# Performance work log

Hardware: AMD Instinct MI355X
Metric: run time of the kernel (lower is better)

The kernel has to match this reference:

```python
import jax, jax.numpy as jnp
import numpy as np

NW1, L1 = 4096, 36
NW2, L2 = 1024, 100
D, NHEAD = 128, 8
HD = D // NHEAD
# alternating full / half-full windows -> exact token count
N1 = (NW1 // 2) * (L1 + L1 // 2)   # 110592
N2 = (NW2 // 2) * (L2 + L2 // 2)   # 76800
N = N1 + N2                        # 187392


def _build_group(nw, L, perm, start):
    """Prefix-valid windows: even windows full (L tokens), odd half (L//2)."""
    lens = np.where(np.arange(nw) % 2 == 0, L, L // 2)
    valid = np.arange(L)[None, :] < lens[:, None]          # [nw, L]
    inds = np.zeros((nw, L), np.int32)
    n = int(lens.sum())
    inds[valid] = perm[start:start + n]                    # row-major prefix fill
    return inds, ~valid, start + n


def setup_inputs() -> dict:
    rng = np.random.default_rng(0)
    perm = rng.permutation(N).astype(np.int32)
    inds1, mask1, ptr = _build_group(NW1, L1, perm, 0)
    inds2, mask2, ptr = _build_group(NW2, L2, perm, ptr)
    assert ptr == N
    ks = jax.random.split(jax.random.key(0), 7)
    scale = 1.0 / np.sqrt(D)
    return {
        "feat_2d": jax.random.normal(ks[0], (N, D), jnp.float32),
        "pos1": jax.random.normal(ks[1], (NW1, L1, D), jnp.float32),
        "pos2": jax.random.normal(ks[2], (NW2, L2, D), jnp.float32),
        "in_proj_w": jax.random.normal(ks[3], (3 * D, D), jnp.float32) * scale,
        "in_proj_b": jax.random.normal(ks[4], (3 * D,), jnp.float32) * 0.02,
        "out_proj_w": jax.random.normal(ks[5], (D, D), jnp.float32) * scale,
        "out_proj_b": jax.random.normal(ks[6], (D,), jnp.float32) * 0.02,
        "inds1": jnp.asarray(inds1),
        "inds2": jnp.asarray(inds2),
        "mask1": jnp.asarray(mask1),
        "mask2": jnp.asarray(mask2),
    }


def _mha(qk, v, pad_mask, Wi, bi, Wo, bo):
    """torch.nn.MultiheadAttention math (eval mode, dropout=0).
    qk, v: [nw, L, D]; pad_mask: [nw, L] True=padded key."""
    nw, L, _ = qk.shape
    q = (qk @ Wi[:D].T + bi[:D]).reshape(nw, L, NHEAD, HD)
    k = (qk @ Wi[D:2 * D].T + bi[D:2 * D]).reshape(nw, L, NHEAD, HD)
    vv = (v @ Wi[2 * D:].T + bi[2 * D:]).reshape(nw, L, NHEAD, HD)
    scores = jnp.einsum('nqhd,nkhd->nhqk', q, k) * (HD ** -0.5)
    scores = jnp.where(pad_mask[:, None, None, :],
                       jnp.finfo(scores.dtype).min, scores)
    attn = jax.nn.softmax(scores, axis=-1)
    out = jnp.einsum('nhqk,nkhd->nqhd', attn, vv).reshape(nw, L, D)
    return out @ Wo.T + bo


def reference(feat_2d, pos1, pos2, in_proj_w, in_proj_b, out_proj_w,
              out_proj_b, inds1, inds2, mask1, mask2):
    out = jnp.zeros_like(feat_2d)
    for inds, mask, pos in ((inds1, mask1, pos1), (inds2, mask2, pos2)):
        f = feat_2d[inds]                      # flat2window gather [nw, L, D]
        o = _mha(f + pos, f, mask,
                 in_proj_w, in_proj_b, out_proj_w, out_proj_b)
        o = o * (~mask)[..., None]             # zero padded slots
        out = out.at[inds.reshape(-1)].add(o.reshape(-1, D))  # window2flat
    return out
```

## Files before the change

### kernel.cpp

```cpp
#include <hip/hip_runtime.h>

typedef __attribute__((ext_vector_type(4))) float f32x4;
typedef __attribute__((ext_vector_type(8))) short short8;
typedef __attribute__((ext_vector_type(4))) short short4v;

#define MFMA_B16(a,b,c) __builtin_amdgcn_mfma_f32_16x16x32_bf16((a),(b),(c),0,0,0)

static __device__ __forceinline__ unsigned short f2bf(float x){
  unsigned int u = __float_as_uint(x);
  u += 0x7fffu + ((u >> 16) & 1u);
  return (unsigned short)(u >> 16);
}

static __device__ __forceinline__ short8 pack8(f32x4 a, f32x4 b){
  short8 r;
  r[0]=(short)f2bf(a[0]); r[1]=(short)f2bf(a[1]); r[2]=(short)f2bf(a[2]); r[3]=(short)f2bf(a[3]);
  r[4]=(short)f2bf(b[0]); r[5]=(short)f2bf(b[1]); r[6]=(short)f2bf(b[2]); r[7]=(short)f2bf(b[3]);
  return r;
}

static __device__ __forceinline__ short4v pack4(const f32x4& a){
  short4v r;
  r[0]=(short)f2bf(a[0]); r[1]=(short)f2bf(a[1]); r[2]=(short)f2bf(a[2]); r[3]=(short)f2bf(a[3]);
  return r;
}

__global__ void prep_w(const float* __restrict__ ipw, const float* __restrict__ opw,
                       unsigned short* __restrict__ wbf){
  int i = blockIdx.x * 256 + threadIdx.x;
  float v = (i < 384*128) ? ipw[i] : opw[i - 384*128];
  wbf[i] = f2bf(v);
}

#define STR 136

template<int TTP>
__global__ __launch_bounds__(256, 2)
void fused_attn(const float* __restrict__ feat,
                const float* __restrict__ pos,
                const int* __restrict__ inds,
                int LW,
                const unsigned short* __restrict__ wqkv,
                const unsigned short* __restrict__ wout,
                const float* __restrict__ ipb, const float* __restrict__ opb,
                float* __restrict__ out)
{
  constexpr int PSTR = 16*(TTP+1) + 8;
  constexpr int STRT = 24;
  constexpr int KOFF = 16*TTP;
  extern __shared__ __align__(16) unsigned short smem[];
  unsigned short* sQK = smem;
  unsigned short* sF  = smem + 16*TTP*STR;
  unsigned short* sPb = smem + 2*16*TTP*STR;
  unsigned short* sTs = smem + 2*16*TTP*STR + 4*16*PSTR;

  const int w = blockIdx.x;
  const int Lv = (w & 1) ? (LW >> 1) : LW;
  const int T  = (Lv + 15) >> 4;
  const long ibase = (long)w * LW;
  const int tid = threadIdx.x;
  const int wv = tid >> 6, lane = tid & 63, c = lane & 15, q = lane >> 4;
  const short8 Z8 = {0,0,0,0,0,0,0,0};
  const f32x4  Z4 = {0.f,0.f,0.f,0.f};

  {
    const int rg = tid >> 4, ch = tid & 15;
    #pragma unroll
    for (int s = 0; s < TTP; ++s){
      if (s < T){
        const int row = s*16 + rg;
        short8 fv = Z8, qv = Z8;
        if (row < Lv){
          const int tok = inds[ibase + row];
          const float* fr = feat + (long)tok*128 + ch*8;
          const float* pr = pos + (ibase + row)*128 + ch*8;
          f32x4 f0 = *(const f32x4*)fr, f1 = *(const f32x4*)(fr+4);
          f32x4 p0 = *(const f32x4*)pr, p1 = *(const f32x4*)(pr+4);
          fv = pack8(f0, f1); qv = pack8(f0+p0, f1+p1);
        }
        *(short8*)&sF [row*STR + ch*8] = fv;
        *(short8*)&sQK[row*STR + ch*8] = qv;
      }
    }
  }
  __syncthreads();

  unsigned short* Pb = sPb + wv*16*PSTR;
  unsigned short* Ts = sTs + wv*16*STRT;
  short4v of[2][TTP];

  #pragma unroll
  for (int hh = 0; hh < 2; ++hh){
    const int h = wv*2 + hh;
    short8 bQ[4], bK[4], bV[4];
    const unsigned short* wr = wqkv + (h*16 + c)*128 + q*8;
    #pragma unroll
    for (int kk = 0; kk < 4; ++kk){
      bQ[kk] = *(const short8*)(wr + kk*32);
      bK[kk] = *(const short8*)(wr + kk*32 + 128*128);
      bV[kk] = *(const short8*)(wr + kk*32 + 2*128*128);
    }
    float bq_r[4], bk_r[4];
    #pragma unroll
    for (int r = 0; r < 4; ++r){
      bq_r[r] = ipb[h*16 + 4*q + r];
      bk_r[r] = ipb[128 + h*16 + 4*q + r];
    }
    const float bv_c = ipb[256 + h*16 + c];

    short8 qAf[TTP], kBf[TTP];

    #pragma unroll
    for (int t = 0; t < TTP; ++t) if (t < T){
      f32x4 qt = Z4, kt = Z4, vt = Z4;
      #pragma unroll
      for (int kk = 0; kk < 4; ++kk){
        const short8 aQ = *(const short8*)&sQK[(16*t + c)*STR + kk*32 + q*8];
        const short8 aF = *(const short8*)&sF [(16*t + c)*STR + kk*32 + q*8];
        qt = MFMA_B16(bQ[kk], aQ, qt);
        kt = MFMA_B16(bK[kk], aQ, kt);
        vt = MFMA_B16(aF, bV[kk], vt);
      }
      #pragma unroll
      for (int r = 0; r < 4; ++r){
        qt[r] = (qt[r] + bq_r[r]) * 0.25f;
        kt[r] += bk_r[r];
        const int key = 16*t + 4*q + r;
        vt[r] = (key < Lv) ? (vt[r] + bv_c) : 0.f;
      }
      *(short4v*)&Pb[c*PSTR + 16*t + 4*q]   = pack4(vt);
      *(short4v*)&Ts[c*STRT + 4*q]          = pack4(qt);
      *(short4v*)&Pb[c*PSTR + KOFF + 4*q]   = pack4(kt);
      const short8 qf = *(const short8*)&Ts[c*STRT + q*8];
      const short8 kf = *(const short8*)&Pb[c*PSTR + KOFF + q*8];
      qAf[t] = (q < 2) ? qf : Z8;
      kBf[t] = (q < 2) ? kf : Z8;
    }
    {
      const short4v z4 = {0,0,0,0};
      *(short4v*)&Pb[c*PSTR + KOFF + 4*q] = z4;
    }

    short8 vBf[(TTP+1)/2];
    #pragma unroll
    for (int u = 0; u < (TTP+1)/2; ++u) if (u < ((T+1)>>1))
      vBf[u] = *(const short8*)&Pb[c*PSTR + 32*u + q*8];

    #pragma unroll
    for (int t = 0; t < TTP; ++t) if (t < T){
      f32x4 St[TTP];
      #pragma unroll
      for (int tk = 0; tk < TTP; ++tk) if (tk < T){
        St[tk] = MFMA_B16(kBf[tk], qAf[t], Z4);
        #pragma unroll
        for (int r = 0; r < 4; ++r){
          const int key = 16*tk + 4*q + r;
          if (key >= Lv) St[tk][r] = -1e30f;
        }
      }
      f32x4 mm = {-1e30f,-1e30f,-1e30f,-1e30f};
      #pragma unroll
      for (int tk = 0; tk < TTP; ++tk) if (tk < T){
        mm[0]=fmaxf(mm[0],St[tk][0]); mm[1]=fmaxf(mm[1],St[tk][1]);
        mm[2]=fmaxf(mm[2],St[tk][2]); mm[3]=fmaxf(mm[3],St[tk][3]);
      }
      float m = fmaxf(fmaxf(mm[0],mm[1]), fmaxf(mm[2],mm[3]));
      m = fmaxf(m, __shfl_xor(m, 16));
      m = fmaxf(m, __shfl_xor(m, 32));
      f32x4 ss = Z4;
      #pragma unroll
      for (int tk = 0; tk < TTP; ++tk) if (tk < T){
        #pragma unroll
        for (int r = 0; r < 4; ++r){
          float e = __expf(St[tk][r] - m);
          St[tk][r] = e; ss[r] += e;
        }
      }
      float sum = (ss[0]+ss[1]) + (ss[2]+ss[3]);
      sum += __shfl_xor(sum, 16);
      sum += __shfl_xor(sum, 32);
      const float inv = 1.0f / sum;
      #pragma unroll
      for (int tk = 0; tk < TTP; ++tk) if (tk < T){
        short4v p4;
        #pragma unroll
        for (int r = 0; r < 4; ++r) p4[r] = (short)f2bf(St[tk][r] * inv);
        *(short4v*)&Pb[c*PSTR + 16*tk + 4*q] = p4;
      }
      f32x4 o = Z4;
      #pragma unroll
      for (int u = 0; u < (TTP+1)/2; ++u) if (u < ((T+1)>>1)){
        const short8 ap = *(const short8*)&Pb[c*PSTR + 32*u + q*8];
        o = MFMA_B16(ap, vBf[u], o);
      }
      short4v ob;
      #pragma unroll
      for (int r = 0; r < 4; ++r) ob[r] = (short)f2bf(o[r]);
      of[hh][t] = ob;
    }
  }

  __syncthreads();
  #pragma unroll
  for (int hh = 0; hh < 2; ++hh){
    const int h = wv*2 + hh;
    #pragma unroll
    for (int t = 0; t < TTP; ++t) if (t < T){
      #pragma unroll
      for (int r = 0; r < 4; ++r)
        sF[(16*t + 4*q + r)*STR + h*16 + c] = (unsigned short)of[hh][t][r];
    }
  }
  __syncthreads();

  float bo_r[8];
  #pragma unroll
  for (int ct = 0; ct < 8; ++ct) bo_r[ct] = opb[ct*16 + c];
  #pragma unroll
  for (int ti = 0; ti < 2; ++ti){
    const int t = wv + ti*4;
    if (t < T){
      f32x4 acc[8];
      #pragma unroll
      for (int ct = 0; ct < 8; ++ct) acc[ct] = Z4;
      #pragma unroll
      for (int p = 0; p < 4; ++p){
        const short8 ao = *(const short8*)&sF[(16*t + c)*STR + p*32 + q*8];
        #pragma unroll
        for (int ct = 0; ct < 8; ++ct){
          const short8 bw = *(const short8*)&wout[(ct*16 + c)*128 + p*32 + q*8];
          acc[ct] = MFMA_B16(ao, bw, acc[ct]);
        }
      }
      #pragma unroll
      for (int r = 0; r < 4; ++r){
        const int l = 16*t + 4*q + r;
        if (l < Lv){
          const int tok = inds[ibase + l];
          float* orow = out + (long)tok*128;
          #pragma unroll
          for (int ct = 0; ct < 8; ++ct)
            orow[ct*16 + c] = acc[ct][r] + bo_r[ct];
        }
      }
    }
  }
}

#define TT3 3
#define PSTR3 (16*(TT3+1) + 8)
#define STRT3 24
#define KOFF3 (16*TT3)
#define HALF3 (2*48*STR + 4*16*PSTR3 + 4*16*STRT3)

__global__ __launch_bounds__(512, 4)
void fused_attn3_2w(const float* __restrict__ feat,
                    const float* __restrict__ pos,
                    const int* __restrict__ inds,
                    const unsigned short* __restrict__ wqkv,
                    const unsigned short* __restrict__ wout,
                    const float* __restrict__ ipb, const float* __restrict__ opb,
                    float* __restrict__ out)
{
  extern __shared__ __align__(16) unsigned short smem[];
  const int tid = threadIdx.x;
  const int wv8 = tid >> 6;
  const int wh  = wv8 >> 2;
  const int wv  = wv8 & 3;
  const int lane = tid & 63, c = lane & 15, q = lane >> 4;

  unsigned short* base = smem + wh*HALF3;
  unsigned short* sQK = base;
  unsigned short* sF  = base + 48*STR;
  unsigned short* sPb = base + 2*48*STR;
  unsigned short* sTs = sPb + 4*16*PSTR3;

  const int w = blockIdx.x*2 + wh;
  const int LW = 36;
  const int Lv = wh ? 18 : 36;
  const int T  = wh ? 2 : 3;
  const long ibase = (long)w * LW;
  const short8 Z8 = {0,0,0,0,0,0,0,0};
  const f32x4  Z4 = {0.f,0.f,0.f,0.f};

  {
    const int ltid = tid & 255;
    const int rg = ltid >> 4, ch = ltid & 15;
    #pragma unroll
    for (int s = 0; s < TT3; ++s){
      if (s < T){
        const int row = s*16 + rg;
        short8 fv = Z8, qv = Z8;
        if (row < Lv){
          const int tok = inds[ibase + row];
          const float* fr = feat + (long)tok*128 + ch*8;
          const float* pr = pos + (ibase + row)*128 + ch*8;
          f32x4 f0 = *(const f32x4*)fr, f1 = *(const f32x4*)(fr+4);
          f32x4 p0 = *(const f32x4*)pr, p1 = *(const f32x4*)(pr+4);
          fv = pack8(f0, f1); qv = pack8(f0+p0, f1+p1);
        }
        *(short8*)&sF [row*STR + ch*8] = fv;
        *(short8*)&sQK[row*STR + ch*8] = qv;
      }
    }
  }
  __syncthreads();

  unsigned short* Pb = sPb + wv*16*PSTR3;
  unsigned short* Ts = sTs + wv*16*STRT3;
  short4v of[2][TT3];

  #pragma unroll
  for (int hh = 0; hh < 2; ++hh){
    const int h = wv*2 + hh;
    short8 bQ[4], bK[4], bV[4];
    const unsigned short* wr = wqkv + (h*16 + c)*128 + q*8;
    #pragma unroll
    for (int kk = 0; kk < 4; ++kk){
      bQ[kk] = *(const short8*)(wr + kk*32);
      bK[kk] = *(const short8*)(wr + kk*32 + 128*128);
      bV[kk] = *(const short8*)(wr + kk*32 + 2*128*128);
    }
    float bq_r[4], bk_r[4];
    #pragma unroll
    for (int r = 0; r < 4; ++r){
      bq_r[r] = ipb[h*16 + 4*q + r];
      bk_r[r] = ipb[128 + h*16 + 4*q + r];
    }
    const float bv_c = ipb[256 + h*16 + c];

    short8 qAf[TT3], kBf[TT3];

    #pragma unroll
    for (int t = 0; t < TT3; ++t) if (t < T){
      f32x4 qt = Z4, kt = Z4, vt = Z4;
      #pragma unroll
      for (int kk = 0; kk < 4; ++kk){
        const short8 aQ = *(const short8*)&sQK[(16*t + c)*STR + kk*32 + q*8];
        const short8 aF = *(const short8*)&sF [(16*t + c)*STR + kk*32 + q*8];
        qt = MFMA_B16(bQ[kk], aQ, qt);
        kt = MFMA_B16(bK[kk], aQ, kt);
        vt = MFMA_B16(aF, bV[kk], vt);
      }
      #pragma unroll
      for (int r = 0; r < 4; ++r){
        qt[r] = (qt[r] + bq_r[r]) * 0.25f;
        kt[r] += bk_r[r];
        const int key = 16*t + 4*q + r;
        vt[r] = (key < Lv) ? (vt[r] + bv_c) : 0.f;
      }
      *(short4v*)&Pb[c*PSTR3 + 16*t + 4*q]   = pack4(vt);
      *(short4v*)&Ts[c*STRT3 + 4*q]          = pack4(qt);
      *(short4v*)&Pb[c*PSTR3 + KOFF3 + 4*q]  = pack4(kt);
      const short8 qf = *(const short8*)&Ts[c*STRT3 + q*8];
      const short8 kf = *(const short8*)&Pb[c*PSTR3 + KOFF3 + q*8];
      qAf[t] = (q < 2) ? qf : Z8;
      kBf[t] = (q < 2) ? kf : Z8;
    }
    {
      const short4v z4 = {0,0,0,0};
      *(short4v*)&Pb[c*PSTR3 + KOFF3 + 4*q] = z4;
    }

    short8 vBf[2];
    #pragma unroll
    for (int u = 0; u < 2; ++u) if (u < ((T+1)>>1))
      vBf[u] = *(const short8*)&Pb[c*PSTR3 + 32*u + q*8];

    #pragma unroll
    for (int t = 0; t < TT3; ++t) if (t < T){
      f32x4 St[TT3];
      #pragma unroll
      for (int tk = 0; tk < TT3; ++tk) if (tk < T){
        St[tk] = MFMA_B16(kBf[tk], qAf[t], Z4);
        #pragma unroll
        for (int r = 0; r < 4; ++r){
          const int key = 16*tk + 4*q + r;
          if (key >= Lv) St[tk][r] = -1e30f;
        }
      }
      f32x4 mm = {-1e30f,-1e30f,-1e30f,-1e30f};
      #pragma unroll
      for (int tk = 0; tk < TT3; ++tk) if (tk < T){
        mm[0]=fmaxf(mm[0],St[tk][0]); mm[1]=fmaxf(mm[1],St[tk][1]);
        mm[2]=fmaxf(mm[2],St[tk][2]); mm[3]=fmaxf(mm[3],St[tk][3]);
      }
      float m = fmaxf(fmaxf(mm[0],mm[1]), fmaxf(mm[2],mm[3]));
      m = fmaxf(m, __shfl_xor(m, 16));
      m = fmaxf(m, __shfl_xor(m, 32));
      f32x4 ss = Z4;
      #pragma unroll
      for (int tk = 0; tk < TT3; ++tk) if (tk < T){
        #pragma unroll
        for (int r = 0; r < 4; ++r){
          float e = __expf(St[tk][r] - m);
          St[tk][r] = e; ss[r] += e;
        }
      }
      float sum = (ss[0]+ss[1]) + (ss[2]+ss[3]);
      sum += __shfl_xor(sum, 16);
      sum += __shfl_xor(sum, 32);
      const float inv = 1.0f / sum;
      #pragma unroll
      for (int tk = 0; tk < TT3; ++tk) if (tk < T){
        short4v p4;
        #pragma unroll
        for (int r = 0; r < 4; ++r) p4[r] = (short)f2bf(St[tk][r] * inv);
        *(short4v*)&Pb[c*PSTR3 + 16*tk + 4*q] = p4;
      }
      f32x4 o = Z4;
      #pragma unroll
      for (int u = 0; u < 2; ++u) if (u < ((T+1)>>1)){
        const short8 ap = *(const short8*)&Pb[c*PSTR3 + 32*u + q*8];
        o = MFMA_B16(ap, vBf[u], o);
      }
      short4v ob;
      #pragma unroll
      for (int r = 0; r < 4; ++r) ob[r] = (short)f2bf(o[r]);
      of[hh][t] = ob;
    }
  }

  __syncthreads();
  #pragma unroll
  for (int hh = 0; hh < 2; ++hh){
    const int h = wv*2 + hh;
    #pragma unroll
    for (int t = 0; t < TT3; ++t) if (t < T){
      #pragma unroll
      for (int r = 0; r < 4; ++r)
        sF[(16*t + 4*q + r)*STR + h*16 + c] = (unsigned short)of[hh][t][r];
    }
  }
  __syncthreads();

  {
    const int t = wv;
    if (t < T){
      float bo_r[8];
      #pragma unroll
      for (int ct = 0; ct < 8; ++ct) bo_r[ct] = opb[ct*16 + c];
      f32x4 acc[8];
      #pragma unroll
      for (int ct = 0; ct < 8; ++ct) acc[ct] = Z4;
      #pragma unroll
      for (int p = 0; p < 4; ++p){
        const short8 ao = *(const short8*)&sF[(16*t + c)*STR + p*32 + q*8];
        #pragma unroll
        for (int ct = 0; ct < 8; ++ct){
          const short8 bw = *(const short8*)&wout[(ct*16 + c)*128 + p*32 + q*8];
          acc[ct] = MFMA_B16(ao, bw, acc[ct]);
        }
      }
      #pragma unroll
      for (int r = 0; r < 4; ++r){
        const int l = 16*t + 4*q + r;
        if (l < Lv){
          const int tok = inds[ibase + l];
          float* orow = out + (long)tok*128;
          #pragma unroll
          for (int ct = 0; ct < 8; ++ct)
            orow[ct*16 + c] = acc[ct][r] + bo_r[ct];
        }
      }
    }
  }
}

extern "C" void kernel_launch(void* const* d_in, const int* in_sizes, int n_in,
                              void* d_out, int out_size, void* d_ws, size_t ws_size,
                              hipStream_t stream) {
  const float* feat = (const float*)d_in[0];
  const float* pos1 = (const float*)d_in[1];
  const float* pos2 = (const float*)d_in[2];
  const float* ipw  = (const float*)d_in[3];
  const float* ipb  = (const float*)d_in[4];
  const float* opw  = (const float*)d_in[5];
  const float* opb  = (const float*)d_in[6];
  const int*   inds1 = (const int*)d_in[7];
  const int*   inds2 = (const int*)d_in[8];
  float* out = (float*)d_out;
  unsigned short* wbf = (unsigned short*)d_ws;
  unsigned short* wob = wbf + 384*128;

  prep_w<<<dim3(256), dim3(256), 0, stream>>>(ipw, opw, wbf);

  {
    const int lds2 = (2*112*STR + 4*16*(16*8 + 8) + 4*16*24) * 2;
    hipFuncSetAttribute((const void*)fused_attn<7>,
                        hipFuncAttributeMaxDynamicSharedMemorySize, lds2);
    fused_attn<7><<<dim3(1024), dim3(256), lds2, stream>>>(
        feat, pos2, inds2, 100, wbf, wob, ipb, opb, out);
  }
  {
    const int lds1 = 2*HALF3*2;
    hipFuncSetAttribute((const void*)fused_attn3_2w,
                        hipFuncAttributeMaxDynamicSharedMemorySize, lds1);
    fused_attn3_2w<<<dim3(2048), dim3(512), lds1, stream>>>(
        feat, pos1, inds1, wbf, wob, ipb, opb, out);
  }
}
```

Baseline: 467.6 us.

## Merge both window-group attention kernels into one launch with block-index dispatch

Combines the L=100 group kernel and the paired L=36 group kernel into a single 512-thread kernel whose block index selects the branch. This removes one launch and the tail gap between the two kernels, so both groups can run concurrently on the device. The L=100 branch now runs with 512 threads, but only four waves do the attention, and it uses the larger shared-memory footprint for every block, which may lower occupancy for the L=36 blocks. Register pressure from the merged code under launch_bounds(512,4) is another risk.

```diff
diff --git a/kernel.cpp b/kernel.cpp
--- a/kernel.cpp
+++ b/kernel.cpp
@@ -34,218 +34,9 @@
 
 #define STR 136
 
-template<int TTP>
-__global__ __launch_bounds__(256, 2)
-void fused_attn(const float* __restrict__ feat,
-                const float* __restrict__ pos,
-                const int* __restrict__ inds,
-                int LW,
-                const unsigned short* __restrict__ wqkv,
-                const unsigned short* __restrict__ wout,
-                const float* __restrict__ ipb, const float* __restrict__ opb,
-                float* __restrict__ out)
-{
-  constexpr int PSTR = 16*(TTP+1) + 8;
-  constexpr int STRT = 24;
-  constexpr int KOFF = 16*TTP;
-  extern __shared__ __align__(16) unsigned short smem[];
-  unsigned short* sQK = smem;
-  unsigned short* sF  = smem + 16*TTP*STR;
-  unsigned short* sPb = smem + 2*16*TTP*STR;
-  unsigned short* sTs = smem + 2*16*TTP*STR + 4*16*PSTR;
-
-  const int w = blockIdx.x;
-  const int Lv = (w & 1) ? (LW >> 1) : LW;
-  const int T  = (Lv + 15) >> 4;
-  const long ibase = (long)w * LW;
-  const int tid = threadIdx.x;
-  const int wv = tid >> 6, lane = tid & 63, c = lane & 15, q = lane >> 4;
-  const short8 Z8 = {0,0,0,0,0,0,0,0};
-  const f32x4  Z4 = {0.f,0.f,0.f,0.f};
-
-  {
-    const int rg = tid >> 4, ch = tid & 15;
-    #pragma unroll
-    for (int s = 0; s < TTP; ++s){
-      if (s < T){
-        const int row = s*16 + rg;
-        short8 fv = Z8, qv = Z8;
-        if (row < Lv){
-          const int tok = inds[ibase + row];
-          const float* fr = feat + (long)tok*128 + ch*8;
-          const float* pr = pos + (ibase + row)*128 + ch*8;
-          f32x4 f0 = *(const f32x4*)fr, f1 = *(const f32x4*)(fr+4);
-          f32x4 p0 = *(const f32x4*)pr, p1 = *(const f32x4*)(pr+4);
-          fv = pack8(f0, f1); qv = pack8(f0+p0, f1+p1);
-        }
-        *(short8*)&sF [row*STR + ch*8] = fv;
-        *(short8*)&sQK[row*STR + ch*8] = qv;
-      }
-    }
-  }
-  __syncthreads();
-
-  unsigned short* Pb = sPb + wv*16*PSTR;
-  unsigned short* Ts = sTs + wv*16*STRT;
-  short4v of[2][TTP];
-
-  #pragma unroll
-  for (int hh = 0; hh < 2; ++hh){
-    const int h = wv*2 + hh;
-    short8 bQ[4], bK[4], bV[4];
-    const unsigned short* wr = wqkv + (h*16 + c)*128 + q*8;
-    #pragma unroll
-    for (int kk = 0; kk < 4; ++kk){
-      bQ[kk] = *(const short8*)(wr + kk*32);
-      bK[kk] = *(const short8*)(wr + kk*32 + 128*128);
-      bV[kk] = *(const short8*)(wr + kk*32 + 2*128*128);
-    }
-    float bq_r[4], bk_r[4];
-    #pragma unroll
-    for (int r = 0; r < 4; ++r){
-      bq_r[r] = ipb[h*16 + 4*q + r];
-      bk_r[r] = ipb[128 + h*16 + 4*q + r];
-    }
-    const float bv_c = ipb[256 + h*16 + c];
-
-    short8 qAf[TTP], kBf[TTP];
-
-    #pragma unroll
-    for (int t = 0; t < TTP; ++t) if (t < T){
-      f32x4 qt = Z4, kt = Z4, vt = Z4;
-      #pragma unroll
-      for (int kk = 0; kk < 4; ++kk){
-        const short8 aQ = *(const short8*)&sQK[(16*t + c)*STR + kk*32 + q*8];
-        const short8 aF = *(const short8*)&sF [(16*t + c)*STR + kk*32 + q*8];
-        qt = MFMA_B16(bQ[kk], aQ, qt);
-        kt = MFMA_B16(bK[kk], aQ, kt);
-        vt = MFMA_B16(aF, bV[kk], vt);
-      }
-      #pragma unroll
-      for (int r = 0; r < 4; ++r){
-        qt[r] = (qt[r] + bq_r[r]) * 0.25f;
-        kt[r] += bk_r[r];
-        const int key = 16*t + 4*q + r;
-        vt[r] = (key < Lv) ? (vt[r] + bv_c) : 0.f;
-      }
-      *(short4v*)&Pb[c*PSTR + 16*t + 4*q]   = pack4(vt);
-      *(short4v*)&Ts[c*STRT + 4*q]          = pack4(qt);
-      *(short4v*)&Pb[c*PSTR + KOFF + 4*q]   = pack4(kt);
-      const short8 qf = *(const short8*)&Ts[c*STRT + q*8];
-      const short8 kf = *(const short8*)&Pb[c*PSTR + KOFF + q*8];
-      qAf[t] = (q < 2) ? qf : Z8;
-      kBf[t] = (q < 2) ? kf : Z8;
-    }
-    {
-      const short4v z4 = {0,0,0,0};
-      *(short4v*)&Pb[c*PSTR + KOFF + 4*q] = z4;
-    }
-
-    short8 vBf[(TTP+1)/2];
-    #pragma unroll
-    for (int u = 0; u < (TTP+1)/2; ++u) if (u < ((T+1)>>1))
-      vBf[u] = *(const short8*)&Pb[c*PSTR + 32*u + q*8];
-
-    #pragma unroll
-    for (int t = 0; t < TTP; ++t) if (t < T){
-      f32x4 St[TTP];
-      #pragma unroll
-      for (int tk = 0; tk < TTP; ++tk) if (tk < T){
-        St[tk] = MFMA_B16(kBf[tk], qAf[t], Z4);
-        #pragma unroll
-        for (int r = 0; r < 4; ++r){
-          const int key = 16*tk + 4*q + r;
-          if (key >= Lv) St[tk][r] = -1e30f;
-        }
-      }
-      f32x4 mm = {-1e30f,-1e30f,-1e30f,-1e30f};
-      #pragma unroll
-      for (int tk = 0; tk < TTP; ++tk) if (tk < T){
-        mm[0]=fmaxf(mm[0],St[tk][0]); mm[1]=fmaxf(mm[1],St[tk][1]);
-        mm[2]=fmaxf(mm[2],St[tk][2]); mm[3]=fmaxf(mm[3],St[tk][3]);
-      }
-      float m = fmaxf(fmaxf(mm[0],mm[1]), fmaxf(mm[2],mm[3]));
-      m = fmaxf(m, __shfl_xor(m, 16));
-      m = fmaxf(m, __shfl_xor(m, 32));
-      f32x4 ss = Z4;
-      #pragma unroll
-      for (int tk = 0; tk < TTP; ++tk) if (tk < T){
-        #pragma unroll
-        for (int r = 0; r < 4; ++r){
-          float e = __expf(St[tk][r] - m);
-          St[tk][r] = e; ss[r] += e;
-        }
-      }
-      float sum = (ss[0]+ss[1]) + (ss[2]+ss[3]);
-      sum += __shfl_xor(sum, 16);
-      sum += __shfl_xor(sum, 32);
-      const float inv = 1.0f / sum;
-      #pragma unroll
-      for (int tk = 0; tk < TTP; ++tk) if (tk < T){
-        short4v p4;
-        #pragma unroll
-        for (int r = 0; r < 4; ++r) p4[r] = (short)f2bf(St[tk][r] * inv);
-        *(short4v*)&Pb[c*PSTR + 16*tk + 4*q] = p4;
-      }
-      f32x4 o = Z4;
-      #pragma unroll
-      for (int u = 0; u < (TTP+1)/2; ++u) if (u < ((T+1)>>1)){
-        const short8 ap = *(const short8*)&Pb[c*PSTR + 32*u + q*8];
-        o = MFMA_B16(ap, vBf[u], o);
-      }
-      short4v ob;
-      #pragma unroll
-      for (int r = 0; r < 4; ++r) ob[r] = (short)f2bf(o[r]);
-      of[hh][t] = ob;
-    }
-  }
-
-  __syncthreads();
-  #pragma unroll
-  for (int hh = 0; hh < 2; ++hh){
-    const int h = wv*2 + hh;
-    #pragma unroll
-    for (int t = 0; t < TTP; ++t) if (t < T){
-      #pragma unroll
-      for (int r = 0; r < 4; ++r)
-        sF[(16*t + 4*q + r)*STR + h*16 + c] = (unsigned short)of[hh][t][r];
-    }
-  }
-  __syncthreads();
-
-  float bo_r[8];
-  #pragma unroll
-  for (int ct = 0; ct < 8; ++ct) bo_r[ct] = opb[ct*16 + c];
-  #pragma unroll
-  for (int ti = 0; ti < 2; ++ti){
-    const int t = wv + ti*4;
-    if (t < T){
-      f32x4 acc[8];
-      #pragma unroll
-      for (int ct = 0; ct < 8; ++ct) acc[ct] = Z4;
-      #pragma unroll
-      for (int p = 0; p < 4; ++p){
-        const short8 ao = *(const short8*)&sF[(16*t + c)*STR + p*32 + q*8];
-        #pragma unroll
-        for (int ct = 0; ct < 8; ++ct){
-          const short8 bw = *(const short8*)&wout[(ct*16 + c)*128 + p*32 + q*8];
-          acc[ct] = MFMA_B16(ao, bw, acc[ct]);
-        }
-      }
-      #pragma unroll
-      for (int r = 0; r < 4; ++r){
-        const int l = 16*t + 4*q + r;
-        if (l < Lv){
-          const int tok = inds[ibase + l];
-          float* orow = out + (long)tok*128;
-          #pragma unroll
-          for (int ct = 0; ct < 8; ++ct)
-            orow[ct*16 + c] = acc[ct][r] + bo_r[ct];
-        }
-      }
-    }
-  }
-}
+#define PSTR2 (16*8 + 8)
+#define STRT2 24
+#define KOFF2 (16*7)
 
 #define TT3 3
 #define PSTR3 (16*(TT3+1) + 8)
@@ -254,213 +45,416 @@
 #define HALF3 (2*48*STR + 4*16*PSTR3 + 4*16*STRT3)
 
 __global__ __launch_bounds__(512, 4)
-void fused_attn3_2w(const float* __restrict__ feat,
-                    const float* __restrict__ pos,
-                    const int* __restrict__ inds,
-                    const unsigned short* __restrict__ wqkv,
-                    const unsigned short* __restrict__ wout,
-                    const float* __restrict__ ipb, const float* __restrict__ opb,
-                    float* __restrict__ out)
+void fused_all(const float* __restrict__ feat,
+               const float* __restrict__ pos1, const float* __restrict__ pos2,
+               const int* __restrict__ inds1, const int* __restrict__ inds2,
+               const unsigned short* __restrict__ wqkv,
+               const unsigned short* __restrict__ wout,
+               const float* __restrict__ ipb, const float* __restrict__ opb,
+               float* __restrict__ out)
 {
   extern __shared__ __align__(16) unsigned short smem[];
+  const int b  = blockIdx.x;
   const int tid = threadIdx.x;
-  const int wv8 = tid >> 6;
-  const int wh  = wv8 >> 2;
-  const int wv  = wv8 & 3;
-  const int lane = tid & 63, c = lane & 15, q = lane >> 4;
-
-  unsigned short* base = smem + wh*HALF3;
-  unsigned short* sQK = base;
-  unsigned short* sF  = base + 48*STR;
-  unsigned short* sPb = base + 2*48*STR;
-  unsigned short* sTs = sPb + 4*16*PSTR3;
-
-  const int w = blockIdx.x*2 + wh;
-  const int LW = 36;
-  const int Lv = wh ? 18 : 36;
-  const int T  = wh ? 2 : 3;
-  const long ibase = (long)w * LW;
   const short8 Z8 = {0,0,0,0,0,0,0,0};
   const f32x4  Z4 = {0.f,0.f,0.f,0.f};
 
-  {
-    const int ltid = tid & 255;
-    const int rg = ltid >> 4, ch = ltid & 15;
+  if (b < 1024){
+    unsigned short* sQK = smem;
+    unsigned short* sF  = smem + 112*STR;
+    unsigned short* sPb = smem + 2*112*STR;
+    unsigned short* sTs = sPb + 4*16*PSTR2;
+
+    const int w  = b;
+    const int Lv = (w & 1) ? 50 : 100;
+    const int T  = (Lv + 15) >> 4;
+    const long ibase = (long)w * 100;
+    const int wv4 = tid >> 6, lane = tid & 63, c = lane & 15, q = lane >> 4;
+
+    {
+      const int rg = tid >> 4, ch = tid & 15;
+      #pragma unroll
+      for (int s = 0; s < 4; ++s){
+        const int row = s*32 + rg;
+        if (row < 16*T){
+          short8 fv = Z8, qv = Z8;
+          if (row < Lv){
+            const int tok = inds2[ibase + row];
+            const float* fr = feat + (long)tok*128 + ch*8;
+            const float* pr = pos2 + (ibase + row)*128 + ch*8;
+            f32x4 f0 = *(const f32x4*)fr, f1 = *(const f32x4*)(fr+4);
+            f32x4 p0 = *(const f32x4*)pr, p1 = *(const f32x4*)(pr+4);
+            fv = pack8(f0, f1); qv = pack8(f0+p0, f1+p1);
+          }
+          *(short8*)&sF [row*STR + ch*8] = fv;
+          *(short8*)&sQK[row*STR + ch*8] = qv;
+        }
+      }
+    }
+    __syncthreads();
+
+    short4v of[2][7];
+    if (wv4 < 4){
+      const int wv = wv4;
+      unsigned short* Pb = sPb + wv*16*PSTR2;
+      unsigned short* Ts = sTs + wv*16*STRT2;
+
+      #pragma unroll
+      for (int hh = 0; hh < 2; ++hh){
+        const int h = wv*2 + hh;
+        short8 bQ[4], bK[4], bV[4];
+        const unsigned short* wr = wqkv + (h*16 + c)*128 + q*8;
+        #pragma unroll
+        for (int kk = 0; kk < 4; ++kk){
+          bQ[kk] = *(const short8*)(wr + kk*32);
+          bK[kk] = *(const short8*)(wr + kk*32 + 128*128);
+          bV[kk] = *(const short8*)(wr + kk*32 + 2*128*128);
+        }
+        float bq_r[4], bk_r[4];
+        #pragma unroll
+        for (int r = 0; r < 4; ++r){
+          bq_r[r] = ipb[h*16 + 4*q + r];
+          bk_r[r] = ipb[128 + h*16 + 4*q + r];
+        }
+        const float bv_c = ipb[256 + h*16 + c];
+
+        short8 qAf[7], kBf[7];
+
+        #pragma unroll
+        for (int t = 0; t < 7; ++t) if (t < T){
+          f32x4 qt = Z4, kt = Z4, vt = Z4;
+          #pragma unroll
+          for (int kk = 0; kk < 4; ++kk){
+            const short8 aQ = *(const short8*)&sQK[(16*t + c)*STR + kk*32 + q*8];
+            const short8 aF = *(const short8*)&sF [(16*t + c)*STR + kk*32 + q*8];
+            qt = MFMA_B16(bQ[kk], aQ, qt);
+            kt = MFMA_B16(bK[kk], aQ, kt);
+            vt = MFMA_B16(aF, bV[kk], vt);
+          }
+          #pragma unroll
+          for (int r = 0; r < 4; ++r){
+            qt[r] = (qt[r] + bq_r[r]) * 0.25f;
+            kt[r] += bk_r[r];
+            const int key = 16*t + 4*q + r;
+            vt[r] = (key < Lv) ? (vt[r] + bv_c) : 0.f;
+          }
+          *(short4v*)&Pb[c*PSTR2 + 16*t + 4*q]   = pack4(vt);
+          *(short4v*)&Ts[c*STRT2 + 4*q]          = pack4(qt);
+          *(short4v*)&Pb[c*PSTR2 + KOFF2 + 4*q]  = pack4(kt);
+          const short8 qf = *(const short8*)&Ts[c*STRT2 + q*8];
+          const short8 kf = *(const short8*)&Pb[c*PSTR2 + KOFF2 + q*8];
+          qAf[t] = (q < 2) ? qf : Z8;
+          kBf[t] = (q < 2) ? kf : Z8;
+        }
+        {
+          const short4v z4 = {0,0,0,0};
+          *(short4v*)&Pb[c*PSTR2 + KOFF2 + 4*q] = z4;
+        }
+
+        short8 vBf[4];
+        #pragma unroll
+        for (int u = 0; u < 4; ++u) if (u < ((T+1)>>1))
+          vBf[u] = *(const short8*)&Pb[c*PSTR2 + 32*u + q*8];
+
+        #pragma unroll
+        for (int t = 0; t < 7; ++t) if (t < T){
+          f32x4 St[7];
+          #pragma unroll
+          for (int tk = 0; tk < 7; ++tk) if (tk < T){
+            St[tk] = MFMA_B16(kBf[tk], qAf[t], Z4);
+            #pragma unroll
+            for (int r = 0; r < 4; ++r){
+              const int key = 16*tk + 4*q + r;
+              if (key >= Lv) St[tk][r] = -1e30f;
+            }
+          }
+          f32x4 mm = {-1e30f,-1e30f,-1e30f,-1e30f};
+          #pragma unroll
+          for (int tk = 0; tk < 7; ++tk) if (tk < T){
+            mm[0]=fmaxf(mm[0],St[tk][0]); mm[1]=fmaxf(mm[1],St[tk][1]);
+            mm[2]=fmaxf(mm[2],St[tk][2]); mm[3]=fmaxf(mm[3],St[tk][3]);
+          }
+          float m = fmaxf(fmaxf(mm[0],mm[1]), fmaxf(mm[2],mm[3]));
+          m = fmaxf(m, __shfl_xor(m, 16));
+          m = fmaxf(m, __shfl_xor(m, 32));
+          f32x4 ss = Z4;
+          #pragma unroll
+          for (int tk = 0; tk < 7; ++tk) if (tk < T){
+            #pragma unroll
+            for (int r = 0; r < 4; ++r){
+              float e = __expf(St[tk][r] - m);
+              St[tk][r] = e; ss[r] += e;
+            }
+          }
+          float sum = (ss[0]+ss[1]) + (ss[2]+ss[3]);
+          sum += __shfl_xor(sum, 16);
+          sum += __shfl_xor(sum, 32);
+          const float inv = 1.0f / sum;
+          #pragma unroll
+          for (int tk = 0; tk < 7; ++tk) if (tk < T){
+            short4v p4;
+            #pragma unroll
+            for (int r = 0; r < 4; ++r) p4[r] = (short)f2bf(St[tk][r] * inv);
+            *(short4v*)&Pb[c*PSTR2 + 16*tk + 4*q] = p4;
+          }
+          f32x4 o = Z4;
+          #pragma unroll
+          for (int u = 0; u < 4; ++u) if (u < ((T+1)>>1)){
+            const short8 ap = *(const short8*)&Pb[c*PSTR2 + 32*u + q*8];
+            o = MFMA_B16(ap, vBf[u], o);
+          }
+          short4v ob;
+          #pragma unroll
+          for (int r = 0; r < 4; ++r) ob[r] = (short)f2bf(o[r]);
+          of[hh][t] = ob;
+        }
+      }
+    }
+
+    __syncthreads();
+    if (wv4 < 4){
+      const int wv = wv4;
+      #pragma unroll
+      for (int hh = 0; hh < 2; ++hh){
+        const int h = wv*2 + hh;
+        #pragma unroll
+        for (int t = 0; t < 7; ++t) if (t < T){
+          #pragma unroll
+          for (int r = 0; r < 4; ++r)
+            sF[(16*t + 4*q + r)*STR + h*16 + c] = (unsigned short)of[hh][t][r];
+        }
+      }
+    }
+    __syncthreads();
+
+    {
+      const int t = wv4;
+      if (t < T){
+        float bo_r[8];
+        #pragma unroll
+        for (int ct = 0; ct < 8; ++ct) bo_r[ct] = opb[ct*16 + c];
+        f32x4 acc[8];
+        #pragma unroll
+        for (int ct = 0; ct < 8; ++ct) acc[ct] = Z4;
+        #pragma unroll
+        for (int p = 0; p < 4; ++p){
+          const short8 ao = *(const short8*)&sF[(16*t + c)*STR + p*32 + q*8];
+          #pragma unroll
+          for (int ct = 0; ct < 8; ++ct){
+            const short8 bw = *(const short8*)&wout[(ct*16 + c)*128 + p*32 + q*8];
+            acc[ct] = MFMA_B16(ao, bw, acc[ct]);
+          }
+        }
+        #pragma unroll
+        for (int r = 0; r < 4; ++r){
+          const int l = 16*t + 4*q + r;
+          if (l < Lv){
+            const int tok = inds2[ibase + l];
+            float* orow = out + (long)tok*128;
+            #pragma unroll
+            for (int ct = 0; ct < 8; ++ct)
+              orow[ct*16 + c] = acc[ct][r] + bo_r[ct];
+          }
+        }
+      }
+    }
+  } else {
+    const int wv8 = tid >> 6;
+    const int wh  = wv8 >> 2;
+    const int wv  = wv8 & 3;
+    const int lane = tid & 63, c = lane & 15, q = lane >> 4;
+
+    unsigned short* base = smem + wh*HALF3;
+    unsigned short* sQK = base;
+    unsigned short* sF  = base + 48*STR;
+    unsigned short* sPb = base + 2*48*STR;
+    unsigned short* sTs = sPb + 4*16*PSTR3;
+
+    const int w = (b - 1024)*2 + wh;
+    const int LW = 36;
+    const int Lv = wh ? 18 : 36;
+    const int T  = wh ? 2 : 3;
+    const long ibase = (long)w * LW;
+
+    {
+      const int ltid = tid & 255;
+      const int rg = ltid >> 4, ch = ltid & 15;
+      #pragma unroll
+      for (int s = 0; s < TT3; ++s){
+        if (s < T){
+          const int row = s*16 + rg;
+          short8 fv = Z8, qv = Z8;
+          if (row < Lv){
+            const int tok = inds1[ibase + row];
+            const float* fr = feat + (long)tok*128 + ch*8;
+            const float* pr = pos1 + (ibase + row)*128 + ch*8;
+            f32x4 f0 = *(const f32x4*)fr, f1 = *(const f32x4*)(fr+4);
+            f32x4 p0 = *(const f32x4*)pr, p1 = *(const f32x4*)(pr+4);
+            fv = pack8(f0, f1); qv = pack8(f0+p0, f1+p1);
+          }
+          *(short8*)&sF [row*STR + ch*8] = fv;
+          *(short8*)&sQK[row*STR + ch*8] = qv;
+        }
+      }
+    }
+    __syncthreads();
+
+    unsigned short* Pb = sPb + wv*16*PSTR3;
+    unsigned short* Ts = sTs + wv*16*STRT3;
+    short4v of[2][TT3];
+
     #pragma unroll
-    for (int s = 0; s < TT3; ++s){
-      if (s < T){
-        const int row = s*16 + rg;
-        short8 fv = Z8, qv = Z8;
-        if (row < Lv){
-          const int tok = inds[ibase + row];
-          const float* fr = feat + (long)tok*128 + ch*8;
-          const float* pr = pos + (ibase + row)*128 + ch*8;
-          f32x4 f0 = *(const f32x4*)fr, f1 = *(const f32x4*)(fr+4);
-          f32x4 p0 = *(const f32x4*)pr, p1 = *(const f32x4*)(pr+4);
-          fv = pack8(f0, f1); qv = pack8(f0+p0, f1+p1);
-        }
-        *(short8*)&sF [row*STR + ch*8] = fv;
-        *(short8*)&sQK[row*STR + ch*8] = qv;
-      }
-    }
-  }
-  __syncthreads();
-
-  unsigned short* Pb = sPb + wv*16*PSTR3;
-  unsigned short* Ts = sTs + wv*16*STRT3;
-  short4v of[2][TT3];
-
-  #pragma unroll
-  for (int hh = 0; hh < 2; ++hh){
-    const int h = wv*2 + hh;
-    short8 bQ[4], bK[4], bV[4];
-    const unsigned short* wr = wqkv + (h*16 + c)*128 + q*8;
+    for (int hh = 0; hh < 2; ++hh){
+      const int h = wv*2 + hh;
+      short8 bQ[4], bK[4], bV[4];
+      const unsigned short* wr = wqkv + (h*16 + c)*128 + q*8;
+      #pragma unroll
+      for (int kk = 0; kk < 4; ++kk){
+        bQ[kk] = *(const short8*)(wr + kk*32);
+        bK[kk] = *(const short8*)(wr + kk*32 + 128*128);
+        bV[kk] = *(const short8*)(wr + kk*32 + 2*128*128);
+      }
+      float bq_r[4], bk_r[4];
+      #pragma unroll
+      for (int r = 0; r < 4; ++r){
+        bq_r[r] = ipb[h*16 + 4*q + r];
+        bk_r[r] = ipb[128 + h*16 + 4*q + r];
+      }
+      const float bv_c = ipb[256 + h*16 + c];
+
+      short8 qAf[TT3], kBf[TT3];
+
+      #pragma unroll
+      for (int t = 0; t < TT3; ++t) if (t < T){
+        f32x4 qt = Z4, kt = Z4, vt = Z4;
+        #pragma unroll
+        for (int kk = 0; kk < 4; ++kk){
+          const short8 aQ = *(const short8*)&sQK[(16*t + c)*STR + kk*32 + q*8];
+          const short8 aF = *(const short8*)&sF [(16*t + c)*STR + kk*32 + q*8];
+          qt = MFMA_B16(bQ[kk], aQ, qt);
+          kt = MFMA_B16(bK[kk], aQ, kt);
+          vt = MFMA_B16(aF, bV[kk], vt);
+        }
+        #pragma unroll
+        for (int r = 0; r < 4; ++r){
+          qt[r] = (qt[r] + bq_r[r]) * 0.25f;
+          kt[r] += bk_r[r];
+          const int key = 16*t + 4*q + r;
+          vt[r] = (key < Lv) ? (vt[r] + bv_c) : 0.f;
+        }
+        *(short4v*)&Pb[c*PSTR3 + 16*t + 4*q]   = pack4(vt);
+        *(short4v*)&Ts[c*STRT3 + 4*q]          = pack4(qt);
+        *(short4v*)&Pb[c*PSTR3 + KOFF3 + 4*q]  = pack4(kt);
+        const short8 qf = *(const short8*)&Ts[c*STRT3 + q*8];
+        const short8 kf = *(const short8*)&Pb[c*PSTR3 + KOFF3 + q*8];
+        qAf[t] = (q < 2) ? qf : Z8;
+        kBf[t] = (q < 2) ? kf : Z8;
+      }
+      {
+        const short4v z4 = {0,0,0,0};
+        *(short4v*)&Pb[c*PSTR3 + KOFF3 + 4*q] = z4;
+      }
+
+      short8 vBf[2];
+      #pragma unroll
+      for (int u = 0; u < 2; ++u) if (u < ((T+1)>>1))
+        vBf[u] = *(const short8*)&Pb[c*PSTR3 + 32*u + q*8];
+
+      #pragma unroll
+      for (int t = 0; t < TT3; ++t) if (t < T){
+        f32x4 St[TT3];
+        #pragma unroll
+        for (int tk = 0; tk < TT3; ++tk) if (tk < T){
+          St[tk] = MFMA_B16(kBf[tk], qAf[t], Z4);
+          #pragma unroll
+          for (int r = 0; r < 4; ++r){
+            const int key = 16*tk + 4*q + r;
+            if (key >= Lv) St[tk][r] = -1e30f;
+          }
+        }
+        f32x4 mm = {-1e30f,-1e30f,-1e30f,-1e30f};
+        #pragma unroll
+        for (int tk = 0; tk < TT3; ++tk) if (tk < T){
+          mm[0]=fmaxf(mm[0],St[tk][0]); mm[1]=fmaxf(mm[1],St[tk][1]);
+          mm[2]=fmaxf(mm[2],St[tk][2]); mm[3]=fmaxf(mm[3],St[tk][3]);
+        }
+        float m = fmaxf(fmaxf(mm[0],mm[1]), fmaxf(mm[2],mm[3]));
+        m = fmaxf(m, __shfl_xor(m, 16));
+        m = fmaxf(m, __shfl_xor(m, 32));
+        f32x4 ss = Z4;
+        #pragma unroll
+        for (int tk = 0; tk < TT3; ++tk) if (tk < T){
+          #pragma unroll
+          for (int r = 0; r < 4; ++r){
+            float e = __expf(St[tk][r] - m);
+            St[tk][r] = e; ss[r] += e;
+          }
+        }
+        float sum = (ss[0]+ss[1]) + (ss[2]+ss[3]);
+        sum += __shfl_xor(sum, 16);
+        sum += __shfl_xor(sum, 32);
+        const float inv = 1.0f / sum;
+        #pragma unroll
+        for (int tk = 0; tk < TT3; ++tk) if (tk < T){
+          short4v p4;
+          #pragma unroll
+          for (int r = 0; r < 4; ++r) p4[r] = (short)f2bf(St[tk][r] * inv);
+          *(short4v*)&Pb[c*PSTR3 + 16*tk + 4*q] = p4;
+        }
+        f32x4 o = Z4;
+        #pragma unroll
+        for (int u = 0; u < 2; ++u) if (u < ((T+1)>>1)){
+          const short8 ap = *(const short8*)&Pb[c*PSTR3 + 32*u + q*8];
+          o = MFMA_B16(ap, vBf[u], o);
+        }
+        short4v ob;
+        #pragma unroll
+        for (int r = 0; r < 4; ++r) ob[r] = (short)f2bf(o[r]);
+        of[hh][t] = ob;
+      }
+    }
+
+    __syncthreads();
     #pragma unroll
-    for (int kk = 0; kk < 4; ++kk){
-      bQ[kk] = *(const short8*)(wr + kk*32);
-      bK[kk] = *(const short8*)(wr + kk*32 + 128*128);
-      bV[kk] = *(const short8*)(wr + kk*32 + 2*128*128);
-    }
-    float bq_r[4], bk_r[4];
-    #pragma unroll
-    for (int r = 0; r < 4; ++r){
-      bq_r[r] = ipb[h*16 + 4*q + r];
-      bk_r[r] = ipb[128 + h*16 + 4*q + r];
-    }
-    const float bv_c = ipb[256 + h*16 + c];
-
-    short8 qAf[TT3], kBf[TT3];
-
-    #pragma unroll
-    for (int t = 0; t < TT3; ++t) if (t < T){
-      f32x4 qt = Z4, kt = Z4, vt = Z4;
-      #pragma unroll
-      for (int kk = 0; kk < 4; ++kk){
-        const short8 aQ = *(const short8*)&sQK[(16*t + c)*STR + kk*32 + q*8];
-        const short8 aF = *(const short8*)&sF [(16*t + c)*STR + kk*32 + q*8];
-        qt = MFMA_B16(bQ[kk], aQ, qt);
-        kt = MFMA_B16(bK[kk], aQ, kt);
-        vt = MFMA_B16(aF, bV[kk], vt);
-      }
-      #pragma unroll
-      for (int r = 0; r < 4; ++r){
-        qt[r] = (qt[r] + bq_r[r]) * 0.25f;
-        kt[r] += bk_r[r];
-        const int key = 16*t + 4*q + r;
-        vt[r] = (key < Lv) ? (vt[r] + bv_c) : 0.f;
-      }
-      *(short4v*)&Pb[c*PSTR3 + 16*t + 4*q]   = pack4(vt);
-      *(short4v*)&Ts[c*STRT3 + 4*q]          = pack4(qt);
-      *(short4v*)&Pb[c*PSTR3 + KOFF3 + 4*q]  = pack4(kt);
-      const short8 qf = *(const short8*)&Ts[c*STRT3 + q*8];
-      const short8 kf = *(const short8*)&Pb[c*PSTR3 + KOFF3 + q*8];
-      qAf[t] = (q < 2) ? qf : Z8;
-      kBf[t] = (q < 2) ? kf : Z8;
-    }
+    for (int hh = 0; hh < 2; ++hh){
+      const int h = wv*2 + hh;
+      #pragma unroll
+      for (int t = 0; t < TT3; ++t) if (t < T){
+        #pragma unroll
+        for (int r = 0; r < 4; ++r)
+          sF[(16*t + 4*q + r)*STR + h*16 + c] = (unsigned short)of[hh][t][r];
+      }
+    }
+    __syncthreads();
+
     {
-      const short4v z4 = {0,0,0,0};
-      *(short4v*)&Pb[c*PSTR3 + KOFF3 + 4*q] = z4;
-    }
-
-    short8 vBf[2];
-    #pragma unroll
-    for (int u = 0; u < 2; ++u) if (u < ((T+1)>>1))
-      vBf[u] = *(const short8*)&Pb[c*PSTR3 + 32*u + q*8];
-
-    #pragma unroll
-    for (int t = 0; t < TT3; ++t) if (t < T){
-      f32x4 St[TT3];
-      #pragma unroll
-      for (int tk = 0; tk < TT3; ++tk) if (tk < T){
-        St[tk] = MFMA_B16(kBf[tk], qAf[t], Z4);
+      const int t = wv;
+      if (t < T){
+        float bo_r[8];
+        #pragma unroll
+        for (int ct = 0; ct < 8; ++ct) bo_r[ct] = opb[ct*16 + c];
+        f32x4 acc[8];
+        #pragma unroll
+        for (int ct = 0; ct < 8; ++ct) acc[ct] = Z4;
+        #pragma unroll
+        for (int p = 0; p < 4; ++p){
+          const short8 ao = *(const short8*)&sF[(16*t + c)*STR + p*32 + q*8];
+          #pragma unroll
+          for (int ct = 0; ct < 8; ++ct){
+            const short8 bw = *(const short8*)&wout[(ct*16 + c)*128 + p*32 + q*8];
+            acc[ct] = MFMA_B16(ao, bw, acc[ct]);
+          }
+        }
         #pragma unroll
         for (int r = 0; r < 4; ++r){
-          const int key = 16*tk + 4*q + r;
-          if (key >= Lv) St[tk][r] = -1e30f;
-        }
-      }
-      f32x4 mm = {-1e30f,-1e30f,-1e30f,-1e30f};
-      #pragma unroll
-      for (int tk = 0; tk < TT3; ++tk) if (tk < T){
-        mm[0]=fmaxf(mm[0],St[tk][0]); mm[1]=fmaxf(mm[1],St[tk][1]);
-        mm[2]=fmaxf(mm[2],St[tk][2]); mm[3]=fmaxf(mm[3],St[tk][3]);
-      }
-      float m = fmaxf(fmaxf(mm[0],mm[1]), fmaxf(mm[2],mm[3]));
-      m = fmaxf(m, __shfl_xor(m, 16));
-      m = fmaxf(m, __shfl_xor(m, 32));
-      f32x4 ss = Z4;
-      #pragma unroll
-      for (int tk = 0; tk < TT3; ++tk) if (tk < T){
-        #pragma unroll
-        for (int r = 0; r < 4; ++r){
-          float e = __expf(St[tk][r] - m);
-          St[tk][r] = e; ss[r] += e;
-        }
-      }
-      float sum = (ss[0]+ss[1]) + (ss[2]+ss[3]);
-      sum += __shfl_xor(sum, 16);
-      sum += __shfl_xor(sum, 32);
-      const float inv = 1.0f / sum;
-      #pragma unroll
-      for (int tk = 0; tk < TT3; ++tk) if (tk < T){
-        short4v p4;
-        #pragma unroll
-        for (int r = 0; r < 4; ++r) p4[r] = (short)f2bf(St[tk][r] * inv);
-        *(short4v*)&Pb[c*PSTR3 + 16*tk + 4*q] = p4;
-      }
-      f32x4 o = Z4;
-      #pragma unroll
-      for (int u = 0; u < 2; ++u) if (u < ((T+1)>>1)){
-        const short8 ap = *(const short8*)&Pb[c*PSTR3 + 32*u + q*8];
-        o = MFMA_B16(ap, vBf[u], o);
-      }
-      short4v ob;
-      #pragma unroll
-      for (int r = 0; r < 4; ++r) ob[r] = (short)f2bf(o[r]);
-      of[hh][t] = ob;
-    }
-  }
-
-  __syncthreads();
-  #pragma unroll
-  for (int hh = 0; hh < 2; ++hh){
-    const int h = wv*2 + hh;
-    #pragma unroll
-    for (int t = 0; t < TT3; ++t) if (t < T){
-      #pragma unroll
-      for (int r = 0; r < 4; ++r)
-        sF[(16*t + 4*q + r)*STR + h*16 + c] = (unsigned short)of[hh][t][r];
-    }
-  }
-  __syncthreads();
-
-  {
-    const int t = wv;
-    if (t < T){
-      float bo_r[8];
-      #pragma unroll
-      for (int ct = 0; ct < 8; ++ct) bo_r[ct] = opb[ct*16 + c];
-      f32x4 acc[8];
-      #pragma unroll
-      for (int ct = 0; ct < 8; ++ct) acc[ct] = Z4;
-      #pragma unroll
-      for (int p = 0; p < 4; ++p){
-        const short8 ao = *(const short8*)&sF[(16*t + c)*STR + p*32 + q*8];
-        #pragma unroll
-        for (int ct = 0; ct < 8; ++ct){
-          const short8 bw = *(const short8*)&wout[(ct*16 + c)*128 + p*32 + q*8];
-          acc[ct] = MFMA_B16(ao, bw, acc[ct]);
-        }
-      }
-      #pragma unroll
-      for (int r = 0; r < 4; ++r){
-        const int l = 16*t + 4*q + r;
-        if (l < Lv){
-          const int tok = inds[ibase + l];
-          float* orow = out + (long)tok*128;
-          #pragma unroll
-          for (int ct = 0; ct < 8; ++ct)
-            orow[ct*16 + c] = acc[ct][r] + bo_r[ct];
+          const int l = 16*t + 4*q + r;
+          if (l < Lv){
+            const int tok = inds1[ibase + l];
+            float* orow = out + (long)tok*128;
+            #pragma unroll
+            for (int ct = 0; ct < 8; ++ct)
+              orow[ct*16 + c] = acc[ct][r] + bo_r[ct];
+          }
         }
       }
     }
@@ -485,18 +479,9 @@
 
   prep_w<<<dim3(256), dim3(256), 0, stream>>>(ipw, opw, wbf);
 
-  {
-    const int lds2 = (2*112*STR + 4*16*(16*8 + 8) + 4*16*24) * 2;
-    hipFuncSetAttribute((const void*)fused_attn<7>,
-                        hipFuncAttributeMaxDynamicSharedMemorySize, lds2);
-    fused_attn<7><<<dim3(1024), dim3(256), lds2, stream>>>(
-        feat, pos2, inds2, 100, wbf, wob, ipb, opb, out);
-  }
-  {
-    const int lds1 = 2*HALF3*2;
-    hipFuncSetAttribute((const void*)fused_attn3_2w,
-                        hipFuncAttributeMaxDynamicSharedMemorySize, lds1);
-    fused_attn3_2w<<<dim3(2048), dim3(512), lds1, stream>>>(
-        feat, pos1, inds1, wbf, wob, ipb, opb, out);
-  }
-}
+  const int lds = (2*112*STR + 4*16*PSTR2 + 4*16*STRT2) * 2;
+  hipFuncSetAttribute((const void*)fused_all,
+                      hipFuncAttributeMaxDynamicSharedMemorySize, lds);
+  fused_all<<<dim3(1024 + 2048), dim3(512), lds, stream>>>(
+      feat, pos1, pos2, inds1, inds2, wbf, wob, ipb, opb, out);
+}
```

Result: faster. 435.0 us (-7.0%).
